# Optimization experiments

Hardware: AMD Instinct MI355X
Metric: run time of the kernel (lower is better)

The kernel has to match this reference:

```python
import jax, jax.numpy as jnp
import numpy as np

# hyperparameters (see init_kwargs)
DP, DS, DO, D, K, C = 256, 256, 64, 320, 10, 10
SI, NS = 100, 22
ALIGN = 0.05
COEF = 0.3989422917366028  # 1/sqrt(2*pi)
B, SEQ, T_STEPS = 32, 512, 200


def _linear_params(key, fan_in, fan_out):
    # torch nn.Linear default init: U(-1/sqrt(fan_in), 1/sqrt(fan_in))
    s = 1.0 / np.sqrt(fan_in)
    kw, kb = jax.random.split(key)
    w = jax.random.uniform(kw, (fan_in, fan_out), minval=-s, maxval=s, dtype=jnp.float32)
    b = jax.random.uniform(kb, (fan_out,), minval=-s, maxval=s, dtype=jnp.float32)
    return w, b


def setup_inputs() -> dict:
    key = jax.random.key(0)
    ks = jax.random.split(key, 8)
    sentence = jax.random.randint(ks[0], (B, SEQ), 0, SI)
    speaker_id = jax.random.randint(ks[1], (B,), 0, NS)
    Lut_P = jax.random.normal(ks[2], (SI, DP), dtype=jnp.float32)
    Lut_S = jax.random.normal(ks[3], (NS, DS), dtype=jnp.float32)
    Na_w, Na_b = _linear_params(ks[4], D * K, 3 * C)
    Nu_w, Nu_b = _linear_params(ks[5], D * K, D)
    No_w, No_b = _linear_params(ks[6], D * K, DO)
    kf = jax.random.split(ks[7], 2)
    Fu_w, Fu_b = _linear_params(kf[0], DS, DP)
    Fo_w, Fo_b = _linear_params(kf[1], DS, D * K)
    return dict(sentence=sentence, speaker_id=speaker_id, Lut_P=Lut_P, Lut_S=Lut_S,
                Na_w=Na_w, Na_b=Na_b, Nu_w=Nu_w, Nu_b=Nu_b, No_w=No_w, No_b=No_b,
                Fu_w=Fu_w, Fu_b=Fu_b, Fo_w=Fo_w, Fo_b=Fo_b, T=T_STEPS)


def reference(sentence, speaker_id, Lut_P, Lut_S, Na_w, Na_b, Nu_w, Nu_b,
              No_w, No_b, Fu_w, Fu_b, Fo_w, Fo_b, T):
    batch, seq_len = sentence.shape
    # Encoder: embedding lookups
    lut_p = Lut_P[sentence]          # (B, S, dp)
    ident = Lut_S[speaker_id]        # (B, ds)

    # ident-dependent terms are loop-invariant; hoist out of the scan
    idt = jnp.tanh(ident @ Fu_w + Fu_b)   # (B, dp)
    fo = ident @ Fo_w + Fo_b              # (B, d*k)

    # initialize(): buffer seeded with speaker embedding in first dp rows
    S0 = jnp.zeros((batch, D, K), dtype=lut_p.dtype)
    S0 = S0.at[:, :DP, :].set(ident[:, :, None])
    mu0 = jnp.zeros((batch, C), dtype=lut_p.dtype)
    o0 = jnp.zeros((batch, DO), dtype=lut_p.dtype)

    J = jnp.arange(1, seq_len + 1, dtype=lut_p.dtype)  # (S,)

    def step(carry, _):
        S_tm1, mu_tm1, o_tm1 = carry
        # --- GMM attention ---
        out = (S_tm1.reshape(batch, D * K) @ Na_w + Na_b).reshape(batch, 3, C)
        k_t, b_t, y_t = out[:, 0], out[:, 1], out[:, 2]
        mu_t = mu_tm1 + ALIGN * jnp.exp(k_t)            # (B, c)
        sig_t = jnp.exp(b_t)                            # (B, c)
        g_t = jax.nn.softmax(y_t, axis=1)               # (B, c)
        # phi: (B, c, S)
        phi = g_t[:, :, None] * jnp.exp(-0.5 * sig_t[:, :, None] * (mu_t[:, :, None] - J) ** 2)
        alpha = COEF * phi.sum(axis=1)                  # (B, S)
        c_t = jnp.einsum('bs,bsd->bd', alpha, lut_p)    # (B, dp)
        # --- Decoder buffer update ---
        C_t = jnp.concatenate([c_t + idt, o_tm1 / 30.0], axis=1)        # (B, d)
        Sp = jnp.concatenate([C_t[:, :, None], S_tm1[:, :, :-1]], axis=2)  # (B, d, k)
        u = Sp.reshape(batch, D * K) @ Nu_w + Nu_b                      # (B, d)
        S_t = jnp.concatenate([u[:, :, None], S_tm1[:, :, :-1]], axis=2)
        o_t = (S_t.reshape(batch, D * K) + fo) @ No_w + No_b            # (B, do)
        return (S_t, mu_t, o_t), o_t

    (_, _, _), outs = jax.lax.scan(step, (S0, mu0, o0), None, length=T)
    return outs  # (T, B, do)
```

## Files before the change

### kernel.cpp

```cpp
#include <hip/hip_runtime.h>

#define DP   256
#define DD   320
#define KK   10
#define CC   10
#define DOUT 64
#define SEQn 512
#define BB   32
#define SI   100
#define NSL  32
#define NGR  8
#define BPG  4
#define NTH  640
#define DPS  10
#define RPS  100

#define PSA   448
#define UF_O  0
#define ZA_O  40
#define ZO_O  168
#define HALF_A (NGR*NSL*PSA)
#define PSB   320
#define CF_OFF 240000

typedef float f4 __attribute__((ext_vector_type(4)));

__device__ __forceinline__ void llc_ld(f4* dst, const float* p) {
    f4 r;
    asm volatile("global_load_dwordx4 %0, %1, off sc0 sc1" : "=&v"(r) : "v"(p));
    asm volatile("s_waitcnt vmcnt(0)" ::: "memory");
    __builtin_amdgcn_sched_barrier(0);
    *dst = r;
}
__device__ __forceinline__ void llc_st(float* p, f4 v) {
    asm volatile("global_store_dwordx4 %0, %1, off sc0 sc1" :: "v"(p), "v"(v) : "memory");
}

__global__ void prep_kernel(int* ctr) {
    if (threadIdx.x < 256) {
        ctr[threadIdx.x] = 0;
        ctr[CF_OFF + threadIdx.x] = 0;
    }
}

__device__ __forceinline__ void gbar(int* c, int target) {
    asm volatile("s_waitcnt vmcnt(0)" ::: "memory");
    __syncthreads();
    if (threadIdx.x == 0) {
        __hip_atomic_fetch_add(c, 1, __ATOMIC_RELEASE, __HIP_MEMORY_SCOPE_AGENT);
        while (__hip_atomic_load(c, __ATOMIC_RELAXED, __HIP_MEMORY_SCOPE_AGENT) < target)
            __builtin_amdgcn_s_sleep(2);
    }
    __syncthreads();
}

__global__ __launch_bounds__(NTH) void recur_kernel(
    const int* __restrict__ sentence, const int* __restrict__ speaker,
    const float* __restrict__ LutP, const float* __restrict__ LutS,
    const float* __restrict__ NaW,  const float* __restrict__ NaB,
    const float* __restrict__ NuW,  const float* __restrict__ NuB,
    const float* __restrict__ NoW,  const float* __restrict__ NoB,
    const float* __restrict__ FuW,  const float* __restrict__ FuB,
    const float* __restrict__ FoW,  const float* __restrict__ FoB,
    float* __restrict__ ws, const int* __restrict__ Tptr,
    float* __restrict__ out)
{
    const int tid  = threadIdx.x;
    const int s    = blockIdx.x & (NSL - 1);
    const int g    = blockIdx.x >> 5;
    const bool owner = (s < BPG);
    const int dbase = s * DPS;
    const int rbase = s * RPS;
    int*  ctr  = (int*)ws + g * 32;
    int*  CFg  = (int*)ws + CF_OFF + g * 32;
    float* pubA = ws + 256;
    float* pubB = ws + 256 + 2 * HALF_A;

    const int c_   = tid >> 6;
    const int lane = tid & 63;

    __shared__ float xsE[BPG][3328];
    __shared__ float wNa[RPS][32];
    __shared__ float wNo[RPS][65];
    __shared__ float naT0[DPS][32];
    __shared__ float noT0[DPS][65];
    __shared__ float identsh[BPG][DP];
    __shared__ float ufull[BPG][DD];
    __shared__ float colL[BPG][DD];
    __shared__ float ucol[BPG*DPS];
    __shared__ float zr[BPG*32];
    __shared__ float zor[BPG*DOUT];
    __shared__ float zastage[NSL][32];
    __shared__ float zostage[NSL][DOUT];
    __shared__ float fos[BPG][RPS];
    __shared__ float nubO[DPS];
    __shared__ float nabL[32];
    __shared__ float aoutL[32];
    __shared__ float muL[CC], sgL[CC], ggL[CC];
    __shared__ float alphaL[SEQn];
    __shared__ float histL[SI];
    __shared__ float idtF[DP];
    __shared__ float colF[DD];
    __shared__ float o_own[DOUT];
    __shared__ float foNoL[DOUT];
    __shared__ int   sentL[SEQn];
    __shared__ int   posidx[SEQn];
    __shared__ int   vstart[SI + 1];
    __shared__ int   vcnt[SI];

    for (int i = tid; i < RPS * 30; i += NTH) {
        int r = i / 30, c = i % 30;
        wNa[r][c] = NaW[(rbase + r) * 30 + c];
    }
    for (int i = tid; i < RPS * 64; i += NTH) {
        int r = i / 64, o = i % 64;
        wNo[r][o] = NoW[(rbase + r) * 64 + o];
    }
    if (tid < DPS * 30) { int dl = tid / 30, c = tid % 30; naT0[dl][c] = NaW[((dbase + dl) * KK) * 30 + c]; }
    if (tid < DPS * 64) { int dl = tid >> 6, o = tid & 63; noT0[dl][o] = NoW[((dbase + dl) * KK) * 64 + o]; }
    if (tid < DPS) nubO[tid] = NuB[dbase + tid];
    if (tid >= 16 && tid < 48) { int c = tid - 16; nabL[c] = (c < 30) ? NaB[c] : 0.f; }
    for (int i = tid; i < BPG * DP; i += NTH) {
        int j = i / DP, v = i % DP;
        identsh[j][v] = LutS[speaker[g * BPG + j] * DP + v];
    }
    __syncthreads();

    float w[50];
    #pragma unroll
    for (int q = 0; q < 50; ++q)
        w[q] = NuW[(size_t)(lane * 50 + q) * DD + dbase + c_];

    for (int i = tid; i < BPG * RPS; i += NTH) {
        int j = i / RPS, r = i % RPS;
        float acc = FoB[rbase + r];
        for (int v = 0; v < DP; v += 8) {
            float wv[8];
            #pragma unroll
            for (int e = 0; e < 8; ++e) wv[e] = FoW[(v + e) * 3200 + rbase + r];
            #pragma unroll
            for (int e = 0; e < 8; ++e) acc += identsh[j][v + e] * wv[e];
        }
        fos[j][r] = acc;
    }
    if (owner) {
        if (tid < DP) {
            float acc = FuB[tid];
            for (int v = 0; v < DP; v += 8) {
                float wv[8];
                #pragma unroll
                for (int e = 0; e < 8; ++e) wv[e] = FuW[(v + e) * DP + tid];
                #pragma unroll
                for (int e = 0; e < 8; ++e) acc += identsh[s][v + e] * wv[e];
            }
            idtF[tid] = tanhf(acc);
        }
        if (tid >= 512 && tid < 512 + CC) muL[tid - 512] = 0.f;
        if (tid < SEQn) sentL[tid] = sentence[(g * BPG + s) * SEQn + tid];
        __syncthreads();
        if (tid < SI) { int cnt = 0; for (int q = 0; q < SEQn; ++q) if (sentL[q] == tid) ++cnt; vcnt[tid] = cnt; }
        __syncthreads();
        if (tid == 0) { int run = 0; for (int v = 0; v < SI; ++v) { vstart[v] = run; run += vcnt[v]; } vstart[SI] = run; }
        __syncthreads();
        if (tid < SI) { int k = vstart[tid]; for (int q = 0; q < SEQn; ++q) if (sentL[q] == tid) posidx[k++] = q; }
    }
    for (int i = tid; i < BPG * 3200; i += NTH) {
        int j = i / 3200, row = i % 3200;
        int d = row / KK;
        xsE[j][(row / 50) * 52 + (row % 50)] = (d < DP) ? identsh[j][d] : 0.f;
    }
    __syncthreads();
    if (tid < 128) {
        int j = tid >> 5, c = tid & 31;
        float acc = 0.f;
        if (c < 30)
            for (int rr = 0; rr < RPS; ++rr) {
                int row = rbase + rr;
                acc += xsE[j][(row / 50) * 52 + (row % 50)] * wNa[rr][c];
            }
        zr[j * 32 + c] = acc;
    }
    if (tid >= 128 && tid < 384) {
        int t = tid - 128, j = t >> 6, o = t & 63;
        float acc = 0.f;
        for (int rr = 0; rr < RPS; ++rr) acc += fos[j][rr] * wNo[rr][o];
        zor[j * 64 + o] = acc;
    }
    __syncthreads();
    {
        float* pa0 = pubA + (size_t)(g * NSL + s) * PSA;
        if (tid < 32) llc_st(pa0 + ZA_O + tid * 4, *(f4*)&zr[tid * 4]);
        if (tid >= 32 && tid < 96) { int q = tid - 32; llc_st(pa0 + ZO_O + q * 4, *(f4*)&zor[q * 4]); }
    }
    gbar(ctr, 32 * 1);

    const int T = Tptr[0];

    for (int i = 0; i < T; ++i) {
        const int rh = i & 1, wh = rh ^ 1;
        float* pa_r = pubA + (size_t)rh * HALF_A + (size_t)g * NSL * PSA;
        float* pa_w = pubA + (size_t)wh * HALF_A + (size_t)(g * NSL + s) * PSA;

        if (i > 0 && tid < 320) {
            int p = tid / 10, q = tid % 10;
            f4 v; llc_ld(&v, pa_r + p * PSA + UF_O + q * 4);
            #pragma unroll
            for (int e = 0; e < 4; ++e) {
                int f = q * 4 + e;
                ufull[f / 10][p * 10 + (f % 10)] = v[e];
            }
        }
        __syncthreads();

        if (owner) {
            f4 v_za = {0.f,0.f,0.f,0.f}, v_zo = {0.f,0.f,0.f,0.f};
            if (tid < 256) {
                const float* p = pa_r + (tid >> 3) * PSA + ZA_O + s * 32 + (tid & 7) * 4;
                asm volatile("global_load_dwordx4 %0, %1, off sc0 sc1" : "=&v"(v_za) : "v"(p));
            }
            if (tid < 512) {
                const float* p = pa_r + (tid >> 4) * PSA + ZO_O + s * 64 + (tid & 15) * 4;
                asm volatile("global_load_dwordx4 %0, %1, off sc0 sc1" : "=&v"(v_zo) : "v"(p));
            }
            asm volatile("s_waitcnt vmcnt(0)" ::: "memory");
            __builtin_amdgcn_sched_barrier(0);
            if (tid < 256) *(f4*)&zastage[tid >> 3][(tid & 7) * 4] = v_za;
            if (tid < 512) *(f4*)&zostage[tid >> 4][(tid & 15) * 4] = v_zo;
            __syncthreads();
            if (tid < 30) {
                float a = nabL[tid];
                for (int p = 0; p < NSL; ++p) a += zastage[p][tid];
                aoutL[tid] = a;
            }
            if (tid >= 64 && tid < 128) {
                int o = tid - 64;
                float v = 0.f;
                for (int p = 0; p < NSL; ++p) v += zostage[p][o];
                if (i == 0) { foNoL[o] = NoB[o] + v; o_own[o] = 0.f; }
                else        o_own[o] = foNoL[o] + v;
            }
            __syncthreads();
            if (tid < CC) {
                muL[tid] += 0.05f * expf(aoutL[tid]);
                sgL[tid] = expf(aoutL[10 + tid]);
                float m = -1e30f;
                for (int q = 0; q < CC; ++q) m = fmaxf(m, aoutL[20 + q]);
                float ssum = 0.f;
                for (int q = 0; q < CC; ++q) ssum += expf(aoutL[20 + q] - m);
                ggL[tid] = expf(aoutL[20 + tid] - m) / ssum;
            }
            __syncthreads();
            if (tid < SEQn) {
                float J = (float)(tid + 1);
                float a = 0.f;
                #pragma unroll
                for (int c = 0; c < CC; ++c) { float dm = muL[c] - J; a += ggL[c] * __expf(-0.5f * sgL[c] * dm * dm); }
                alphaL[tid] = a * 0.3989422917366028f;
            }
            __syncthreads();
            if (tid < SI) {
                float h = 0.f;
                for (int k = vstart[tid]; k < vstart[tid + 1]; ++k) h += alphaL[posidx[k]];
                histL[tid] = h;
            }
            __syncthreads();
            if (tid < DP) {
                float acc = idtF[tid];
                for (int v = 0; v < SI; v += 10) {
                    float wv[10];
                    #pragma unroll
                    for (int e = 0; e < 10; ++e) wv[e] = LutP[(v + e) * DP + tid];
                    #pragma unroll
                    for (int e = 0; e < 10; ++e) acc += histL[v + e] * wv[e];
                }
                colF[tid] = acc;
            } else if (tid < DD) {
                colF[tid] = o_own[tid - DP] * (1.0f / 30.0f);
            }
            __syncthreads();
            if (i > 0 && tid < DOUT)
                out[((size_t)(i - 1) * BB + (g * BPG + s)) * DOUT + tid] = o_own[tid];
            if (tid < 80) llc_st(pubB + (size_t)(g * BPG + s) * PSB + tid * 4, *(f4*)&colF[tid * 4]);
            asm volatile("s_waitcnt vmcnt(0)" ::: "memory");
            __syncthreads();
            if (tid == 0)
                __hip_atomic_store(&CFg[s], i + 1, __ATOMIC_RELEASE, __HIP_MEMORY_SCOPE_AGENT);
        }

        for (int it = tid; it < BPG * DD; it += NTH) {
            int j = it / DD, d = it % DD;
            float* p = &xsE[j][(d / 5) * 52 + (d % 5) * 10];
            float t0 = p[0];
            float v1 = p[1], v2 = p[2], v3 = p[3], v4 = p[4], v5 = p[5], v6 = p[6], v7 = p[7], v8 = p[8];
            p[1] = (i == 0) ? t0 : ufull[j][d];
            p[2] = v1; p[3] = v2; p[4] = v3; p[5] = v4; p[6] = v5; p[7] = v6; p[8] = v7; p[9] = v8;
        }
        if (tid < BPG) {
            while (__hip_atomic_load(&CFg[tid], __ATOMIC_RELAXED, __HIP_MEMORY_SCOPE_AGENT) < i + 1)
                __builtin_amdgcn_s_sleep(2);
        }
        __syncthreads();

        if (tid < 320) {
            int j = tid / 80, q = tid % 80;
            f4 v; llc_ld(&v, pubB + (size_t)(g * BPG + j) * PSB + q * 4);
            #pragma unroll
            for (int e = 0; e < 4; ++e) colL[j][q * 4 + e] = v[e];
        }
        __syncthreads();
        for (int it = tid; it < BPG * DD; it += NTH) {
            int j = it / DD, d = it % DD;
            xsE[j][(d / 5) * 52 + (d % 5) * 10] = colL[j][d];
        }
        __syncthreads();

        {
            float accE[BPG];
            #pragma unroll
            for (int j = 0; j < BPG; ++j) {
                const float* xb = &xsE[j][lane * 52];
                float a = 0.f;
                #pragma unroll
                for (int qq = 0; qq < 12; ++qq) {
                    f4 x = *(const f4*)(xb + qq * 4);
                    a += x.x * w[qq * 4] + x.y * w[qq * 4 + 1] + x.z * w[qq * 4 + 2] + x.w * w[qq * 4 + 3];
                }
                a += xb[48] * w[48] + xb[49] * w[49];
                accE[j] = a;
            }
            #pragma unroll
            for (int j = 0; j < BPG; ++j)
                for (int off = 32; off; off >>= 1) accE[j] += __shfl_xor(accE[j], off, 64);
            if (lane == 0) {
                #pragma unroll
                for (int j = 0; j < BPG; ++j) ucol[j * DPS + c_] = accE[j] + nubO[c_];
            }
        }
        __syncthreads();

        if (tid < 128) {
            int j = tid >> 5, c = tid & 31;
            float acc = 0.f;
            if (c < 30) {
                for (int dd = 0; dd < DPS; ++dd) {
                    int rg = 2 * s + (dd >= 5);
                    int of = dd * 10 - (dd >= 5 ? 50 : 0);
                    const float* xb = &xsE[j][rg * 52 + of];
                    #pragma unroll
                    for (int k = 1; k < KK; ++k) acc += xb[k] * wNa[dd * 10 + k][c];
                }
                #pragma unroll
                for (int dl = 0; dl < DPS; ++dl) acc += ucol[j * DPS + dl] * naT0[dl][c];
            }
            zr[j * 32 + c] = acc;
        }
        if (tid >= 128 && tid < 384) {
            int t = tid - 128, j = t >> 6, o = t & 63;
            float acc = 0.f;
            for (int dd = 0; dd < DPS; ++dd) {
                int rg = 2 * s + (dd >= 5);
                int of = dd * 10 - (dd >= 5 ? 50 : 0);
                const float* xb = &xsE[j][rg * 52 + of];
                #pragma unroll
                for (int k = 1; k < KK; ++k) acc += xb[k] * wNo[dd * 10 + k][o];
            }
            #pragma unroll
            for (int dl = 0; dl < DPS; ++dl) acc += ucol[j * DPS + dl] * noT0[dl][o];
            zor[j * 64 + o] = acc;
        }
        __syncthreads();

        if (tid < 10)                llc_st(pa_w + UF_O + tid * 4,        *(f4*)&ucol[tid * 4]);
        if (tid >= 10 && tid < 42)  { int q = tid - 10; llc_st(pa_w + ZA_O + q * 4, *(f4*)&zr[q * 4]); }
        if (tid >= 42 && tid < 106) { int q = tid - 42; llc_st(pa_w + ZO_O + q * 4, *(f4*)&zor[q * 4]); }
        gbar(ctr, 32 * (i + 2));
    }

    if (owner) {
        const float* pa_r = pubA + (size_t)(T & 1) * HALF_A + (size_t)g * NSL * PSA;
        if (tid < 512) {
            f4 v; llc_ld(&v, pa_r + (tid >> 4) * PSA + ZO_O + s * 64 + (tid & 15) * 4);
            *(f4*)&zostage[tid >> 4][(tid & 15) * 4] = v;
        }
        __syncthreads();
        if (tid < DOUT) {
            float v = foNoL[tid];
            for (int p = 0; p < NSL; ++p) v += zostage[p][tid];
            out[((size_t)(T - 1) * BB + (g * BPG + s)) * DOUT + tid] = v;
        }
    }
}

extern "C" void kernel_launch(void* const* d_in, const int* in_sizes, int n_in,
                              void* d_out, int out_size, void* d_ws, size_t ws_size,
                              hipStream_t stream) {
    const int*   sentence = (const int*)d_in[0];
    const int*   speaker  = (const int*)d_in[1];
    const float* LutP = (const float*)d_in[2];
    const float* LutS = (const float*)d_in[3];
    const float* NaW  = (const float*)d_in[4];
    const float* NaB  = (const float*)d_in[5];
    const float* NuW  = (const float*)d_in[6];
    const float* NuB  = (const float*)d_in[7];
    const float* NoW  = (const float*)d_in[8];
    const float* NoB  = (const float*)d_in[9];
    const float* FuW  = (const float*)d_in[10];
    const float* FuB  = (const float*)d_in[11];
    const float* FoW  = (const float*)d_in[12];
    const float* FoB  = (const float*)d_in[13];
    const int*   Tptr = (const int*)d_in[14];
    float* ws   = (float*)d_ws;
    float* outp = (float*)d_out;

    hipLaunchKernelGGL(prep_kernel, dim3(1), dim3(256), 0, stream, (int*)d_ws);
    hipLaunchKernelGGL(recur_kernel, dim3(NSL * NGR), dim3(NTH), 0, stream,
                       sentence, speaker, LutP, LutS, NaW, NaB,
                       NuW, NuB, NoW, NoB, FuW, FuB, FoW, FoB,
                       ws, Tptr, outp);
}
```

Baseline: 4.940 ms.

## Precompute context contribution to Nu on owner and defer the cross-block wait

Owner blocks now multiply the new context column by the slice of Nu_w that acts on column 0 and publish the resulting partial u vector, instead of publishing the raw column. Other blocks zero those weights in their register copy, so the column-independent work (the Nu, Na and No partial sums over shifted history) can run before waiting on the owner's flag. After the wait, each block loads only its 10 needed partial values and adds the missing terms. The intent is to move the cross-block dependency later so it overlaps with local work. In exchange the owner does an extra 320x320 matrix-vector product per step, reading Nu_w from global memory, and there are additional barriers.

```diff
diff --git a/kernel.cpp b/kernel.cpp
--- a/kernel.cpp
+++ b/kernel.cpp
@@ -31,6 +31,13 @@
     asm volatile("s_waitcnt vmcnt(0)" ::: "memory");
     __builtin_amdgcn_sched_barrier(0);
     *dst = r;
+}
+__device__ __forceinline__ float llc_ld1(const float* p) {
+    float r;
+    asm volatile("global_load_dword %0, %1, off sc0 sc1" : "=&v"(r) : "v"(p));
+    asm volatile("s_waitcnt vmcnt(0)" ::: "memory");
+    __builtin_amdgcn_sched_barrier(0);
+    return r;
 }
 __device__ __forceinline__ void llc_st(float* p, f4 v) {
     asm volatile("global_store_dwordx4 %0, %1, off sc0 sc1" :: "v"(p), "v"(v) : "memory");
@@ -86,7 +93,6 @@
     __shared__ float noT0[DPS][65];
     __shared__ float identsh[BPG][DP];
     __shared__ float ufull[BPG][DD];
-    __shared__ float colL[BPG][DD];
     __shared__ float ucol[BPG*DPS];
     __shared__ float zr[BPG*32];
     __shared__ float zor[BPG*DOUT];
@@ -101,6 +107,8 @@
     __shared__ float histL[SI];
     __shared__ float idtF[DP];
     __shared__ float colF[DD];
+    __shared__ float duL[DD];
+    __shared__ float dupart[2*DD];
     __shared__ float o_own[DOUT];
     __shared__ float foNoL[DOUT];
     __shared__ int   sentL[SEQn];
@@ -128,8 +136,10 @@
 
     float w[50];
     #pragma unroll
-    for (int q = 0; q < 50; ++q)
-        w[q] = NuW[(size_t)(lane * 50 + q) * DD + dbase + c_];
+    for (int q = 0; q < 50; ++q) {
+        int r = lane * 50 + q;
+        w[q] = (q % 10 == 0) ? 0.f : NuW[(size_t)r * DD + dbase + c_];
+    }
 
     for (int i = tid; i < BPG * RPS; i += NTH) {
         int j = i / RPS, r = i % RPS;
@@ -280,7 +290,24 @@
             __syncthreads();
             if (i > 0 && tid < DOUT)
                 out[((size_t)(i - 1) * BB + (g * BPG + s)) * DOUT + tid] = o_own[tid];
-            if (tid < 80) llc_st(pubB + (size_t)(g * BPG + s) * PSB + tid * 4, *(f4*)&colF[tid * 4]);
+            {
+                int half = tid / 320, c2 = tid % 320;
+                float a = 0.f;
+                for (int q = 0; q < 160; q += 8) {
+                    float wv[8], xv[8];
+                    #pragma unroll
+                    for (int e = 0; e < 8; ++e) wv[e] = NuW[(size_t)(10 * (half * 160 + q + e)) * DD + c2];
+                    #pragma unroll
+                    for (int e = 0; e < 8; ++e) xv[e] = colF[half * 160 + q + e];
+                    #pragma unroll
+                    for (int e = 0; e < 8; ++e) a += xv[e] * wv[e];
+                }
+                dupart[half * DD + c2] = a;
+            }
+            __syncthreads();
+            if (tid < DD) duL[tid] = dupart[tid] + dupart[DD + tid];
+            __syncthreads();
+            if (tid < 80) llc_st(pubB + (size_t)(g * BPG + s) * PSB + tid * 4, *(f4*)&duL[tid * 4]);
             asm volatile("s_waitcnt vmcnt(0)" ::: "memory");
             __syncthreads();
             if (tid == 0)
@@ -295,23 +322,6 @@
             p[1] = (i == 0) ? t0 : ufull[j][d];
             p[2] = v1; p[3] = v2; p[4] = v3; p[5] = v4; p[6] = v5; p[7] = v6; p[8] = v7; p[9] = v8;
         }
-        if (tid < BPG) {
-            while (__hip_atomic_load(&CFg[tid], __ATOMIC_RELAXED, __HIP_MEMORY_SCOPE_AGENT) < i + 1)
-                __builtin_amdgcn_s_sleep(2);
-        }
-        __syncthreads();
-
-        if (tid < 320) {
-            int j = tid / 80, q = tid % 80;
-            f4 v; llc_ld(&v, pubB + (size_t)(g * BPG + j) * PSB + q * 4);
-            #pragma unroll
-            for (int e = 0; e < 4; ++e) colL[j][q * 4 + e] = v[e];
-        }
-        __syncthreads();
-        for (int it = tid; it < BPG * DD; it += NTH) {
-            int j = it / DD, d = it % DD;
-            xsE[j][(d / 5) * 52 + (d % 5) * 10] = colL[j][d];
-        }
         __syncthreads();
 
         {
@@ -333,7 +343,7 @@
                 for (int off = 32; off; off >>= 1) accE[j] += __shfl_xor(accE[j], off, 64);
             if (lane == 0) {
                 #pragma unroll
-                for (int j = 0; j < BPG; ++j) ucol[j * DPS + c_] = accE[j] + nubO[c_];
+                for (int j = 0; j < BPG; ++j) ucol[j * DPS + c_] = accE[j];
             }
         }
         __syncthreads();
@@ -349,8 +359,6 @@
                     #pragma unroll
                     for (int k = 1; k < KK; ++k) acc += xb[k] * wNa[dd * 10 + k][c];
                 }
-                #pragma unroll
-                for (int dl = 0; dl < DPS; ++dl) acc += ucol[j * DPS + dl] * naT0[dl][c];
             }
             zr[j * 32 + c] = acc;
         }
@@ -364,9 +372,38 @@
                 #pragma unroll
                 for (int k = 1; k < KK; ++k) acc += xb[k] * wNo[dd * 10 + k][o];
             }
-            #pragma unroll
-            for (int dl = 0; dl < DPS; ++dl) acc += ucol[j * DPS + dl] * noT0[dl][o];
             zor[j * 64 + o] = acc;
+        }
+        __syncthreads();
+
+        if (tid < BPG) {
+            while (__hip_atomic_load(&CFg[tid], __ATOMIC_RELAXED, __HIP_MEMORY_SCOPE_AGENT) < i + 1)
+                __builtin_amdgcn_s_sleep(2);
+        }
+        __syncthreads();
+
+        if (tid < BPG * DPS) {
+            int j = tid / DPS, dl = tid % DPS;
+            float duv = llc_ld1(pubB + (size_t)(g * BPG + j) * PSB + dbase + dl);
+            ucol[j * DPS + dl] += duv + nubO[dl];
+        }
+        __syncthreads();
+
+        if (tid < 128) {
+            int j = tid >> 5, c = tid & 31;
+            if (c < 30) {
+                float a = 0.f;
+                #pragma unroll
+                for (int dl = 0; dl < DPS; ++dl) a += ucol[j * DPS + dl] * naT0[dl][c];
+                zr[j * 32 + c] += a;
+            }
+        }
+        if (tid >= 128 && tid < 384) {
+            int t = tid - 128, j = t >> 6, o = t & 63;
+            float a = 0.f;
+            #pragma unroll
+            for (int dl = 0; dl < DPS; ++dl) a += ucol[j * DPS + dl] * noT0[dl][o];
+            zor[j * 64 + o] += a;
         }
         __syncthreads();
 
```

New measurement: 5.634 ms. 1.14x slower.
